# Kernel tuning notes

Measured on AMD Instinct MI355X. Metric: run time of the kernel, lower is better.

Reference implementation:

```python
import jax, jax.numpy as jnp
import numpy as np

N_HEAD = 16


def setup_inputs() -> dict:
    key = jax.random.key(0)
    ks = jax.random.split(key, 6)
    B, S, D = 2, 2048, 1024
    w = 0.02
    return {
        "x": jax.random.normal(ks[0], (B, S, D), dtype=jnp.float32),
        "attention_mask": jnp.ones((B, S), dtype=jnp.int32),
        "Wq": jax.random.normal(ks[1], (D, D), dtype=jnp.float32) * w,
        "bq": jnp.zeros((D,), dtype=jnp.float32),
        "Wk": jax.random.normal(ks[2], (D, D), dtype=jnp.float32) * w,
        "bk": jnp.zeros((D,), dtype=jnp.float32),
        "Wv": jax.random.normal(ks[3], (D, D), dtype=jnp.float32) * w,
        "bv": jnp.zeros((D,), dtype=jnp.float32),
        "Wp": jax.random.normal(ks[4], (D, D), dtype=jnp.float32) * w,
        "bp": jnp.zeros((D,), dtype=jnp.float32),
    }


def reference(x, attention_mask, Wq, bq, Wk, bk, Wv, bv, Wp, bp):
    # x: (B,S,D); PyTorch Linear: y = x @ W.T + b
    B, S, D = x.shape
    H = N_HEAD
    HD = D // H
    scale = 1.0 / jnp.sqrt(jnp.asarray(HD, dtype=x.dtype))

    def heads(W, b):
        return (x @ W.T + b).reshape(B, S, H, HD).transpose(0, 2, 1, 3)  # (B,H,S,HD)

    q = heads(Wq, bq)
    k = heads(Wk, bk)
    v = heads(Wv, bv)

    logits = jnp.einsum("bhsd,bhtd->bhst", q, k) * scale  # (B,H,S,S)

    causal = jnp.tril(jnp.ones((S, S), dtype=bool))  # (S,S)
    am = attention_mask.astype(bool)
    mask = causal[None, None, :, :] & (am[:, None, :, None] & am[:, None, None, :])

    float_min = jnp.finfo(x.dtype).min
    logits = jnp.where(mask, logits, float_min)
    w = jax.nn.softmax(logits, axis=-1)  # dropout is identity in eval / p=0

    attn = jnp.einsum("bhst,bhtd->bhsd", w, v)  # (B,H,S,HD)
    attn = attn.transpose(0, 2, 1, 3).reshape(B, S, D)
    return attn @ Wp.T + bp
```

## Files before the change

### kernel.cpp

```cpp
#include <hip/hip_runtime.h>


#define BB 2
#define SS 2048
#define DD 1024
#define HH 16
#define HDD 64
#define NEG_BIG (-1.0e30f)
#define QSCL 0.18033688011112042f

typedef __attribute__((ext_vector_type(8))) short short8;
typedef __attribute__((ext_vector_type(4))) float floatx4;
typedef unsigned int u32;
#define AS_GLOBAL __attribute__((address_space(1)))
#define AS_LDS    __attribute__((address_space(3)))

__device__ __forceinline__ ushort f2bf(float f) {
    unsigned u = __float_as_uint(f);
    u += 0x7fffu + ((u >> 16) & 1u);
    return (ushort)(u >> 16);
}
__device__ __forceinline__ unsigned pk2(float a, float b) {
    return ((unsigned)f2bf(b) << 16) | (unsigned)f2bf(a);
}
__device__ __forceinline__ unsigned cvtpk(float a, float b) {
    unsigned r;
    asm("v_cvt_pk_bf16_f32 %0, %1, %2" : "=v"(r) : "v"(a), "v"(b));
    return r;
}
__device__ __forceinline__ void unpack8(const uint4 u, float* d) {
    d[0] = __uint_as_float(u.x << 16);
    d[1] = __uint_as_float(u.x & 0xffff0000u);
    d[2] = __uint_as_float(u.y << 16);
    d[3] = __uint_as_float(u.y & 0xffff0000u);
    d[4] = __uint_as_float(u.z << 16);
    d[5] = __uint_as_float(u.z & 0xffff0000u);
    d[6] = __uint_as_float(u.w << 16);
    d[7] = __uint_as_float(u.w & 0xffff0000u);
}
__device__ __forceinline__ void dma16(void* lds, const void* g) {
    __builtin_amdgcn_global_load_lds((const AS_GLOBAL u32*)g, (AS_LDS u32*)lds,
                                     16, 0, 0);
}
__device__ __forceinline__ void bar() {
    asm volatile("s_waitcnt lgkmcnt(0)" ::: "memory");
    __builtin_amdgcn_s_barrier();
    asm volatile("" ::: "memory");
}

__global__ __launch_bounds__(256) void cvt_all(
    const float* __restrict__ x, const float* __restrict__ wq,
    const float* __restrict__ wk, const float* __restrict__ wv,
    const float* __restrict__ wp,
    ushort* __restrict__ dst, ushort* __restrict__ wp_dst)
{
    const size_t flat = ((size_t)blockIdx.x * 256 + threadIdx.x) * 8;
    const float* s;
    ushort* d = dst + flat;
    size_t off;
    float scl = 1.0f;
    if (flat < (size_t)4194304)      { s = x;  off = flat; }
    else if (flat < (size_t)5242880) { s = wq; off = flat - 4194304; scl = QSCL; }
    else if (flat < (size_t)6291456) { s = wk; off = flat - 5242880; }
    else if (flat < (size_t)7340032) { s = wv; off = flat - 6291456; }
    else { s = wp; off = flat - 7340032; d = wp_dst + off; }
    const float4 a = ((const float4*)(s + off))[0];
    const float4 b = ((const float4*)(s + off))[1];
    uint4 u;
    u.x = pk2(a.x * scl, a.y * scl); u.y = pk2(a.z * scl, a.w * scl);
    u.z = pk2(b.x * scl, b.y * scl); u.w = pk2(b.z * scl, b.w * scl);
    *(uint4*)d = u;
}

__global__ __launch_bounds__(256, 3) void gemm_qkv_t34(
    const ushort* __restrict__ A,
    const ushort* __restrict__ W0, const ushort* __restrict__ W1,
    const ushort* __restrict__ W2,
    const float* __restrict__ B0, const float* __restrict__ B1,
    const float* __restrict__ B2,
    ushort* __restrict__ O0, ushort* __restrict__ O1, ushort* __restrict__ O2)
{
    __shared__ ushort As[2][128 * 32];
    __shared__ ushort Bs[2][128 * 32];
    __shared__ float bias_s[128];

    const int z = blockIdx.z;
    const ushort* W = (z == 0) ? W0 : (z == 1 ? W1 : W2);
    const float* bias = (z == 0) ? B0 : (z == 1 ? B1 : B2);
    ushort* out = (z == 0) ? O0 : (z == 1 ? O1 : O2);
    const bool isv = (z == 2);

    const int tid = threadIdx.x;
    const int bm = blockIdx.x * 128, bn = blockIdx.y * 128;
    const int wave = tid >> 6, lane = tid & 63, quad = lane >> 4, lm = lane & 15;
    const int r0 = tid >> 2, c0 = (tid & 3) * 8;
    const int c0s = ((tid & 3) ^ ((tid >> 3) & 3)) * 8;
    const int csw8 = (quad ^ ((lm >> 1) & 3)) * 8;

    if (tid < 128) {
        float bb = bias[bn + tid];
        if (z == 0) bb *= QSCL;
        bias_s[tid] = bb;
    }

    const floatx4 zz = {0.f, 0.f, 0.f, 0.f};
    floatx4 acc[16];
#pragma unroll
    for (int i = 0; i < 16; ++i) acc[i] = zz;

    const ushort* ap = A + (size_t)(bm + r0) * DD + c0;
    const ushort* wpp = W + (size_t)(bn + r0) * DD + c0;

    uint4 pA0, pA1, pA2, pA3, pB0, pB1, pB2, pB3;

#define LOADS(s, K0)                                              \
    do {                                                          \
        s##0 = *(const uint4*)(ap + (K0));                        \
        s##1 = *(const uint4*)(ap + (size_t)64 * DD + (K0));      \
        s##2 = *(const uint4*)(wpp + (K0));                       \
        s##3 = *(const uint4*)(wpp + (size_t)64 * DD + (K0));     \
    } while (0)
#define STORES(buf, s)                                            \
    do {                                                          \
        *(uint4*)&As[buf][r0 * 32 + c0s] = s##0;                  \
        *(uint4*)&As[buf][(64 + r0) * 32 + c0s] = s##1;           \
        *(uint4*)&Bs[buf][r0 * 32 + c0s] = s##2;                  \
        *(uint4*)&Bs[buf][(64 + r0) * 32 + c0s] = s##3;           \
    } while (0)
#define COMPUTE(buf)                                                          \
    do {                                                                      \
        if (isv) {                                                            \
            const short8 bf0 = *(const short8*)&Bs[buf][(wave * 32 + lm) * 32 + csw8];      \
            const short8 bf1 = *(const short8*)&Bs[buf][(wave * 32 + 16 + lm) * 32 + csw8]; \
            _Pragma("unroll")                                                 \
            for (int i = 0; i < 8; ++i) {                                     \
                const short8 af = *(const short8*)&As[buf][(i * 16 + lm) * 32 + csw8];      \
                acc[i * 2 + 0] = __builtin_amdgcn_mfma_f32_16x16x32_bf16(     \
                    af, bf0, acc[i * 2 + 0], 0, 0, 0);                        \
                acc[i * 2 + 1] = __builtin_amdgcn_mfma_f32_16x16x32_bf16(     \
                    af, bf1, acc[i * 2 + 1], 0, 0, 0);                        \
            }                                                                 \
        } else {                                                              \
            const short8 af0 = *(const short8*)&As[buf][(wave * 32 + lm) * 32 + csw8];      \
            const short8 af1 = *(const short8*)&As[buf][(wave * 32 + 16 + lm) * 32 + csw8]; \
            _Pragma("unroll")                                                 \
            for (int j = 0; j < 8; ++j) {                                     \
                const short8 bf = *(const short8*)&Bs[buf][(j * 16 + lm) * 32 + csw8];      \
                acc[j] = __builtin_amdgcn_mfma_f32_16x16x32_bf16(             \
                    bf, af0, acc[j], 0, 0, 0);                                \
                acc[8 + j] = __builtin_amdgcn_mfma_f32_16x16x32_bf16(         \
                    bf, af1, acc[8 + j], 0, 0, 0);                            \
            }                                                                 \
        }                                                                     \
    } while (0)

    LOADS(pA, 0);
    STORES(0, pA);
    bar();
    LOADS(pA, 32);

    for (int k0 = 0; k0 < DD; k0 += 64) {
        if (k0 + 64 < DD) LOADS(pB, k0 + 64);
        COMPUTE(0);
        STORES(1, pA);
        bar();
        if (k0 + 96 < DD) LOADS(pA, k0 + 96);
        COMPUTE(1);
        if (k0 + 64 < DD) STORES(0, pB);
        bar();
    }
#undef LOADS
#undef STORES
#undef COMPUTE

    if (isv) {
        const int b = bm >> 11, sbase = bm & 2047;
#pragma unroll
        for (int j = 0; j < 2; ++j) {
            const int n = bn + wave * 32 + j * 16 + lm;
            const float bb = bias_s[n - bn];
            ushort* orow = out + ((size_t)(b * DD + n)) * SS;
#pragma unroll
            for (int i = 0; i < 8; ++i) {
                const floatx4 a = acc[i * 2 + j];
                ushort4 v;
                v.x = f2bf(a[0] + bb); v.y = f2bf(a[1] + bb);
                v.z = f2bf(a[2] + bb); v.w = f2bf(a[3] + bb);
                *(ushort4*)(orow + sbase + i * 16 + quad * 4) = v;
            }
        }
    } else {
#pragma unroll
        for (int i = 0; i < 2; ++i) {
            const int m = bm + wave * 32 + i * 16 + lm;
            const int b = m >> 11, s = m & 2047;
#pragma unroll
            for (int j = 0; j < 8; ++j) {
                const int nl = j * 16 + quad * 4;
                const int n = bn + nl;
                const int h = n >> 6, hd = n & 63;
                const floatx4 a = acc[i * 8 + j];
                ushort4 v;
                v.x = f2bf(a[0] + bias_s[nl + 0]);
                v.y = f2bf(a[1] + bias_s[nl + 1]);
                v.z = f2bf(a[2] + bias_s[nl + 2]);
                v.w = f2bf(a[3] + bias_s[nl + 3]);
                *(ushort4*)(out + (((size_t)(b * HH + h) * SS) + s) * HDD + hd) = v;
            }
        }
    }
}

__global__ __launch_bounds__(256, 2) void gemm_proj_t34(
    const ushort* __restrict__ A, const ushort* __restrict__ W,
    const float* __restrict__ bias, float* __restrict__ out)
{
    __shared__ ushort As[2][128 * 32];
    __shared__ ushort Bs[2][128 * 32];
    __shared__ float bias_s[128];

    const int tid = threadIdx.x;
    const int bm = blockIdx.x * 128, bn = blockIdx.y * 128;
    const int wave = tid >> 6, lane = tid & 63, quad = lane >> 4, lm = lane & 15;
    const int wm = wave >> 1, wn = wave & 1;
    const int r0 = tid >> 2, c0 = (tid & 3) * 8;
    const int c0s = ((tid & 3) ^ ((tid >> 3) & 3)) * 8;
    const int csw8 = (quad ^ ((lm >> 1) & 3)) * 8;

    if (tid < 128) bias_s[tid] = bias[bn + tid];

    const floatx4 zz = {0.f, 0.f, 0.f, 0.f};
    floatx4 acc[4][4];
#pragma unroll
    for (int i = 0; i < 4; ++i)
#pragma unroll
        for (int j = 0; j < 4; ++j) acc[i][j] = zz;

    const ushort* ap = A + (size_t)(bm + r0) * DD + c0;
    const ushort* wpp = W + (size_t)(bn + r0) * DD + c0;

    uint4 pA0, pA1, pA2, pA3, pB0, pB1, pB2, pB3;

#define LOADS(s, K0)                                              \
    do {                                                          \
        s##0 = *(const uint4*)(ap + (K0));                        \
        s##1 = *(const uint4*)(ap + (size_t)64 * DD + (K0));      \
        s##2 = *(const uint4*)(wpp + (K0));                       \
        s##3 = *(const uint4*)(wpp + (size_t)64 * DD + (K0));     \
    } while (0)
#define STORES(buf, s)                                            \
    do {                                                          \
        *(uint4*)&As[buf][r0 * 32 + c0s] = s##0;                  \
        *(uint4*)&As[buf][(64 + r0) * 32 + c0s] = s##1;           \
        *(uint4*)&Bs[buf][r0 * 32 + c0s] = s##2;                  \
        *(uint4*)&Bs[buf][(64 + r0) * 32 + c0s] = s##3;           \
    } while (0)
#define COMPUTE(buf)                                                          \
    do {                                                                      \
        short8 af[4], bf[4];                                                  \
        _Pragma("unroll")                                                     \
        for (int i = 0; i < 4; ++i)                                           \
            af[i] = *(const short8*)&As[buf][(wm * 64 + i * 16 + lm) * 32 + csw8]; \
        _Pragma("unroll")                                                     \
        for (int j = 0; j < 4; ++j)                                           \
            bf[j] = *(const short8*)&Bs[buf][(wn * 64 + j * 16 + lm) * 32 + csw8]; \
        _Pragma("unroll")                                                     \
        for (int i = 0; i < 4; ++i)                                           \
            _Pragma("unroll")                                                 \
            for (int j = 0; j < 4; ++j)                                       \
                acc[i][j] = __builtin_amdgcn_mfma_f32_16x16x32_bf16(          \
                    bf[j], af[i], acc[i][j], 0, 0, 0);                        \
    } while (0)

    LOADS(pA, 0);
    STORES(0, pA);
    bar();
    LOADS(pA, 32);

    for (int k0 = 0; k0 < DD; k0 += 64) {
        if (k0 + 64 < DD) LOADS(pB, k0 + 64);
        COMPUTE(0);
        STORES(1, pA);
        bar();
        if (k0 + 96 < DD) LOADS(pA, k0 + 96);
        COMPUTE(1);
        if (k0 + 64 < DD) STORES(0, pB);
        bar();
    }
#undef LOADS
#undef STORES
#undef COMPUTE

#pragma unroll
    for (int i = 0; i < 4; ++i) {
#pragma unroll
        for (int j = 0; j < 4; ++j) {
            const int nl = wn * 64 + j * 16 + quad * 4;
            const int n = bn + nl;
            const int m = bm + wm * 64 + i * 16 + lm;
            float4 v;
            v.x = acc[i][j][0] + bias_s[nl + 0];
            v.y = acc[i][j][1] + bias_s[nl + 1];
            v.z = acc[i][j][2] + bias_s[nl + 2];
            v.w = acc[i][j][3] + bias_s[nl + 3];
            *(float4*)(out + (size_t)m * DD + n) = v;
        }
    }
}

__global__ __launch_bounds__(256) void attn_mfma(
    const ushort* __restrict__ Q, const ushort* __restrict__ K,
    const ushort* __restrict__ Vt, const int* __restrict__ am,
    ushort* __restrict__ Opart, float* __restrict__ lbuf)
{
    __shared__ ushort Ks[64 * 72];
    __shared__ ushort Vts[64 * 72];
    __shared__ ushort Ps[4][16 * 72];
    __shared__ int amk_s[64];

    const int tid = threadIdx.x;
    const int wq = tid >> 6, lane = tid & 63, quad = lane >> 4, lm = lane & 15;
    const int bh = blockIdx.y, b = bh >> 4, h = bh & 15;
    const int pslot = (int)blockIdx.x;
    const int split = (int)blockIdx.z;
    const size_t base = (size_t)bh * SS * HDD;
    const size_t tbase = (size_t)bh * HDD * SS;
    const int* amrow = am + b * SS;
    const int sr = tid >> 2, sc = (tid & 3) * 16;
    const floatx4 zz = {0.f, 0.f, 0.f, 0.f};

#pragma unroll
    for (int ph = 0; ph < 2; ++ph) {
        const int qt64 = ph ? (31 - pslot) : pslot;
        const int q0 = qt64 * 64;
        const int ktend = qt64;
        const int qrow = q0 + wq * 16 + lm;

        if (ph) __syncthreads();

        short8 qf0, qf1;
        {
            const ushort* qp = Q + base + (size_t)qrow * HDD + quad * 8;
            qf0 = *(const short8*)qp;
            qf1 = *(const short8*)(qp + 32);
        }
        const int amq = amrow[qrow];
        const bool allq = __all(amq != 0);

        floatx4 o_acc[4];
#pragma unroll
        for (int n2 = 0; n2 < 4; ++n2) o_acc[n2] = zz;
        float l_lane = 0.f;

        if (split <= ktend) {
            uint4 kra, krb, vra, vrb;
            int amr = 1;
            {
                const ushort* kp = K + base + (size_t)(split * 64 + sr) * HDD + sc;
                kra = ((const uint4*)kp)[0]; krb = ((const uint4*)kp)[1];
                const ushort* vp = Vt + tbase + (size_t)sr * SS + split * 64 + sc;
                vra = ((const uint4*)vp)[0]; vrb = ((const uint4*)vp)[1];
                if (tid < 64) amr = amrow[split * 64 + tid];
            }
            *(uint4*)&Ks[sr * 72 + sc] = kra;
            *(uint4*)&Ks[sr * 72 + sc + 8] = krb;
            *(uint4*)&Vts[sr * 72 + sc] = vra;
            *(uint4*)&Vts[sr * 72 + sc + 8] = vrb;
            if (tid < 64) amk_s[tid] = amr;
            __syncthreads();

            for (int kt = split; kt <= ktend; kt += 2) {
                const int nxt = kt + 2;
                const bool have_nxt = nxt <= ktend;
                if (have_nxt) {
                    const ushort* kp = K + base + (size_t)(nxt * 64 + sr) * HDD + sc;
                    kra = ((const uint4*)kp)[0]; krb = ((const uint4*)kp)[1];
                    const ushort* vp = Vt + tbase + (size_t)sr * SS + nxt * 64 + sc;
                    vra = ((const uint4*)vp)[0]; vrb = ((const uint4*)vp)[1];
                    if (tid < 64) amr = amrow[nxt * 64 + tid];
                }

                const bool allk = (__ballot(amk_s[lane] != 0) == ~0ull);
                const bool fast = allk & allq & ((kt * 64 + 63) <= (q0 + wq * 16));
                if (fast) {
#pragma unroll
                    for (int nt = 0; nt < 4; ++nt) {
                        const short8 kf0 = *(const short8*)&Ks[(nt * 16 + lm) * 72 + quad * 8];
                        const short8 kf1 = *(const short8*)&Ks[(nt * 16 + lm) * 72 + 32 + quad * 8];
                        floatx4 s = zz;
                        s = __builtin_amdgcn_mfma_f32_16x16x32_bf16(kf0, qf0, s, 0, 0, 0);
                        s = __builtin_amdgcn_mfma_f32_16x16x32_bf16(kf1, qf1, s, 0, 0, 0);
                        const float e0 = exp2f(s[0]);
                        const float e1 = exp2f(s[1]);
                        const float e2 = exp2f(s[2]);
                        const float e3 = exp2f(s[3]);
                        l_lane += (e0 + e1) + (e2 + e3);
                        uint2 pv;
                        pv.x = cvtpk(e0, e1); pv.y = cvtpk(e2, e3);
                        *(uint2*)&Ps[wq][lm * 72 + nt * 16 + quad * 4] = pv;
                    }
                } else {
#pragma unroll
                    for (int nt = 0; nt < 4; ++nt) {
                        const short8 kf0 = *(const short8*)&Ks[(nt * 16 + lm) * 72 + quad * 8];
                        const short8 kf1 = *(const short8*)&Ks[(nt * 16 + lm) * 72 + 32 + quad * 8];
                        const int4 amk4 = *(const int4*)&amk_s[nt * 16 + quad * 4];
                        floatx4 s = zz;
                        s = __builtin_amdgcn_mfma_f32_16x16x32_bf16(kf0, qf0, s, 0, 0, 0);
                        s = __builtin_amdgcn_mfma_f32_16x16x32_bf16(kf1, qf1, s, 0, 0, 0);
                        const int t0 = kt * 64 + nt * 16 + quad * 4;
                        const bool mq = amq != 0;
                        const bool ok0 = amk4.x && mq && (t0 + 0 <= qrow);
                        const bool ok1 = amk4.y && mq && (t0 + 1 <= qrow);
                        const bool ok2 = amk4.z && mq && (t0 + 2 <= qrow);
                        const bool ok3 = amk4.w && mq && (t0 + 3 <= qrow);
                        const float e0 = exp2f(ok0 ? s[0] : NEG_BIG);
                        const float e1 = exp2f(ok1 ? s[1] : NEG_BIG);
                        const float e2 = exp2f(ok2 ? s[2] : NEG_BIG);
                        const float e3 = exp2f(ok3 ? s[3] : NEG_BIG);
                        l_lane += (e0 + e1) + (e2 + e3);
                        uint2 pv;
                        pv.x = cvtpk(e0, e1); pv.y = cvtpk(e2, e3);
                        *(uint2*)&Ps[wq][lm * 72 + nt * 16 + quad * 4] = pv;
                    }
                }

                const short8 af0 = *(const short8*)&Ps[wq][lm * 72 + quad * 8];
                const short8 af1 = *(const short8*)&Ps[wq][lm * 72 + 32 + quad * 8];
#pragma unroll
                for (int n2 = 0; n2 < 4; ++n2) {
                    const short8 vf0 = *(const short8*)&Vts[(n2 * 16 + lm) * 72 + quad * 8];
                    const short8 vf1 = *(const short8*)&Vts[(n2 * 16 + lm) * 72 + 32 + quad * 8];
                    o_acc[n2] = __builtin_amdgcn_mfma_f32_16x16x32_bf16(
                        vf0, af0, o_acc[n2], 0, 0, 0);
                    o_acc[n2] = __builtin_amdgcn_mfma_f32_16x16x32_bf16(
                        vf1, af1, o_acc[n2], 0, 0, 0);
                }

                if (have_nxt) {
                    __syncthreads();
                    *(uint4*)&Ks[sr * 72 + sc] = kra;
                    *(uint4*)&Ks[sr * 72 + sc + 8] = krb;
                    *(uint4*)&Vts[sr * 72 + sc] = vra;
                    *(uint4*)&Vts[sr * 72 + sc + 8] = vrb;
                    if (tid < 64) amk_s[tid] = amr;
                    __syncthreads();
                }
            }
        }

        float l = l_lane;
        l += __shfl_xor(l, 16);
        l += __shfl_xor(l, 32);
        if (quad == 0)
            lbuf[(size_t)split * (BB * HH * SS) + (size_t)bh * SS + qrow] = l;
#pragma unroll
        for (int n2 = 0; n2 < 4; ++n2) {
            uint2 v;
            v.x = cvtpk(o_acc[n2][0], o_acc[n2][1]);
            v.y = cvtpk(o_acc[n2][2], o_acc[n2][3]);
            *(uint2*)(Opart + (size_t)split * (BB * SS * DD)
                        + ((size_t)(b * SS + qrow)) * DD + h * HDD + n2 * 16 + quad * 4) = v;
        }
    }
}

__global__ __launch_bounds__(256) void combine(
    const ushort* __restrict__ Opart, const float* __restrict__ lbuf,
    ushort* __restrict__ Aout)
{
    const size_t e = ((size_t)blockIdx.x * 256 + threadIdx.x) * 8;
    const int m = (int)(e >> 10);
    const int col = (int)(e & 1023);
    const int b = m >> 11, s = m & 2047, h = col >> 6;
    const float l = lbuf[(b * HH + h) * SS + s]
                  + lbuf[BB * HH * SS + (b * HH + h) * SS + s];
    const float inv = l > 0.f ? 1.f / l : 0.f;
    const uint4 u0 = *(const uint4*)(Opart + e);
    const uint4 u1 = *(const uint4*)(Opart + (size_t)BB * SS * DD + e);
    float f0[8], f1[8];
    unpack8(u0, f0);
    unpack8(u1, f1);
    uint4 o;
    o.x = pk2((f0[0] + f1[0]) * inv, (f0[1] + f1[1]) * inv);
    o.y = pk2((f0[2] + f1[2]) * inv, (f0[3] + f1[3]) * inv);
    o.z = pk2((f0[4] + f1[4]) * inv, (f0[5] + f1[5]) * inv);
    o.w = pk2((f0[6] + f1[6]) * inv, (f0[7] + f1[7]) * inv);
    *(uint4*)(Aout + e) = o;
}

extern "C" void kernel_launch(void* const* d_in, const int* in_sizes, int n_in,
                              void* d_out, int out_size, void* d_ws, size_t ws_size,
                              hipStream_t stream) {
    const float* x  = (const float*)d_in[0];
    const int*   am = (const int*)d_in[1];
    const float* Wq = (const float*)d_in[2];
    const float* bq = (const float*)d_in[3];
    const float* Wk = (const float*)d_in[4];
    const float* bk = (const float*)d_in[5];
    const float* Wv = (const float*)d_in[6];
    const float* bv = (const float*)d_in[7];
    const float* Wp = (const float*)d_in[8];
    const float* bp = (const float*)d_in[9];
    float* out = (float*)d_out;

    const size_t elems = (size_t)BB * HH * SS * HDD;
    ushort* q_ws = (ushort*)d_ws;
    ushort* k_ws = q_ws + elems;
    ushort* v_ws = k_ws + elems;
    float*  lbuf = (float*)(v_ws + elems);
    ushort* wpb  = (ushort*)(lbuf + 2 * BB * HH * SS);

    ushort* xb  = (ushort*)d_out;
    ushort* wqb = xb + 4194304;
    ushort* wkb = wqb + 1048576;
    ushort* wvb = wkb + 1048576;

    cvt_all<<<4096, 256, 0, stream>>>(x, Wq, Wk, Wv, Wp, xb, wpb);

    gemm_qkv_t34<<<dim3(32, 8, 3), 256, 0, stream>>>(
        xb, wqb, wkb, wvb, bq, bk, bv, q_ws, k_ws, v_ws);

    attn_mfma<<<dim3(16, BB * HH, 2), 256, 0, stream>>>(
        q_ws, k_ws, v_ws, am, (ushort*)d_out, lbuf);

    combine<<<2048, 256, 0, stream>>>((const ushort*)d_out, lbuf, q_ws);

    gemm_proj_t34<<<dim3(32, 8), 256, 0, stream>>>(q_ws, wpb, bp, out);
}
```

Measured before the change: 250.4 us.

## Replace double-buffered LDS pipeline in projection GEMM with single-buffer register staging

The output projection GEMM drops its two LDS buffers and two register prefetch sets in favour of a single LDS buffer. The next K-slice is prefetched into registers while the current one is computed, and two barriers per 32-wide K step guard the LDS overwrite. This halves LDS use and trims register pressure, but doubles the barrier count and removes overlap between the LDS stores and MFMA work. The QKV GEMM's launch-bounds occupancy hint is also lowered from 3 to 2 blocks per CU.

```diff
diff --git a/kernel.cpp b/kernel.cpp
--- a/kernel.cpp
+++ b/kernel.cpp
@@ -72,7 +72,7 @@
     *(uint4*)d = u;
 }
 
-__global__ __launch_bounds__(256, 3) void gemm_qkv_t34(
+__global__ __launch_bounds__(256, 2) void gemm_qkv_t34(
     const ushort* __restrict__ A,
     const ushort* __restrict__ W0, const ushort* __restrict__ W1,
     const ushort* __restrict__ W2,
@@ -211,12 +211,12 @@
     }
 }
 
-__global__ __launch_bounds__(256, 2) void gemm_proj_t34(
+__global__ __launch_bounds__(256, 2) void gemm_proj_rs(
     const ushort* __restrict__ A, const ushort* __restrict__ W,
     const float* __restrict__ bias, float* __restrict__ out)
 {
-    __shared__ ushort As[2][128 * 32];
-    __shared__ ushort Bs[2][128 * 32];
+    __shared__ ushort As[128 * 32];
+    __shared__ ushort Bs[128 * 32];
     __shared__ float bias_s[128];
 
     const int tid = threadIdx.x;
@@ -239,57 +239,52 @@
     const ushort* ap = A + (size_t)(bm + r0) * DD + c0;
     const ushort* wpp = W + (size_t)(bn + r0) * DD + c0;
 
-    uint4 pA0, pA1, pA2, pA3, pB0, pB1, pB2, pB3;
-
-#define LOADS(s, K0)                                              \
-    do {                                                          \
-        s##0 = *(const uint4*)(ap + (K0));                        \
-        s##1 = *(const uint4*)(ap + (size_t)64 * DD + (K0));      \
-        s##2 = *(const uint4*)(wpp + (K0));                       \
-        s##3 = *(const uint4*)(wpp + (size_t)64 * DD + (K0));     \
+    uint4 ar0, ar1, wr0, wr1;
+#define LOADT(K0)                                                \
+    do {                                                         \
+        ar0 = *(const uint4*)(ap + (K0));                        \
+        ar1 = *(const uint4*)(ap + (size_t)64 * DD + (K0));      \
+        wr0 = *(const uint4*)(wpp + (K0));                       \
+        wr1 = *(const uint4*)(wpp + (size_t)64 * DD + (K0));     \
     } while (0)
-#define STORES(buf, s)                                            \
-    do {                                                          \
-        *(uint4*)&As[buf][r0 * 32 + c0s] = s##0;                  \
-        *(uint4*)&As[buf][(64 + r0) * 32 + c0s] = s##1;           \
-        *(uint4*)&Bs[buf][r0 * 32 + c0s] = s##2;                  \
-        *(uint4*)&Bs[buf][(64 + r0) * 32 + c0s] = s##3;           \
+#define STORET()                                                 \
+    do {                                                         \
+        *(uint4*)&As[r0 * 32 + c0s] = ar0;                       \
+        *(uint4*)&As[(64 + r0) * 32 + c0s] = ar1;                \
+        *(uint4*)&Bs[r0 * 32 + c0s] = wr0;                       \
+        *(uint4*)&Bs[(64 + r0) * 32 + c0s] = wr1;                \
     } while (0)
-#define COMPUTE(buf)                                                          \
-    do {                                                                      \
-        short8 af[4], bf[4];                                                  \
-        _Pragma("unroll")                                                     \
-        for (int i = 0; i < 4; ++i)                                           \
-            af[i] = *(const short8*)&As[buf][(wm * 64 + i * 16 + lm) * 32 + csw8]; \
-        _Pragma("unroll")                                                     \
-        for (int j = 0; j < 4; ++j)                                           \
-            bf[j] = *(const short8*)&Bs[buf][(wn * 64 + j * 16 + lm) * 32 + csw8]; \
-        _Pragma("unroll")                                                     \
-        for (int i = 0; i < 4; ++i)                                           \
-            _Pragma("unroll")                                                 \
-            for (int j = 0; j < 4; ++j)                                       \
-                acc[i][j] = __builtin_amdgcn_mfma_f32_16x16x32_bf16(          \
-                    bf[j], af[i], acc[i][j], 0, 0, 0);                        \
-    } while (0)
-
-    LOADS(pA, 0);
-    STORES(0, pA);
-    bar();
-    LOADS(pA, 32);
-
-    for (int k0 = 0; k0 < DD; k0 += 64) {
-        if (k0 + 64 < DD) LOADS(pB, k0 + 64);
-        COMPUTE(0);
-        STORES(1, pA);
-        bar();
-        if (k0 + 96 < DD) LOADS(pA, k0 + 96);
-        COMPUTE(1);
-        if (k0 + 64 < DD) STORES(0, pB);
-        bar();
+
+    LOADT(0);
+    STORET();
+    __syncthreads();
+
+    for (int k0 = 0; k0 < DD; k0 += 32) {
+        const bool have_nxt = (k0 + 32) < DD;
+        if (have_nxt) LOADT(k0 + 32);
+
+        short8 af[4], bf[4];
+#pragma unroll
+        for (int i = 0; i < 4; ++i)
+            af[i] = *(const short8*)&As[(wm * 64 + i * 16 + lm) * 32 + csw8];
+#pragma unroll
+        for (int j = 0; j < 4; ++j)
+            bf[j] = *(const short8*)&Bs[(wn * 64 + j * 16 + lm) * 32 + csw8];
+#pragma unroll
+        for (int i = 0; i < 4; ++i)
+#pragma unroll
+            for (int j = 0; j < 4; ++j)
+                acc[i][j] = __builtin_amdgcn_mfma_f32_16x16x32_bf16(
+                    bf[j], af[i], acc[i][j], 0, 0, 0);
+
+        if (have_nxt) {
+            __syncthreads();
+            STORET();
+            __syncthreads();
+        }
     }
-#undef LOADS
-#undef STORES
-#undef COMPUTE
+#undef LOADT
+#undef STORET
 
 #pragma unroll
     for (int i = 0; i < 4; ++i) {
@@ -526,5 +521,5 @@
 
     combine<<<2048, 256, 0, stream>>>((const ushort*)d_out, lbuf, q_ws);
 
-    gemm_proj_t34<<<dim3(32, 8), 256, 0, stream>>>(q_ws, wpb, bp, out);
-}
+    gemm_proj_rs<<<dim3(32, 8), 256, 0, stream>>>(q_ws, wpb, bp, out);
+}
```

After: 206.1 us. 1.21x faster.
